# Kernel tuning notes

Measured on AMD Instinct MI355X. Metric: run time of the kernel, lower is better.

## Reference

```python
import jax, jax.numpy as jnp
import numpy as np

HID, NBINS = 256, 4
NMIR, NMRNA, B, NP, PD = 2000, 20000, 16, 2048, 1024
EREG, EPM, EPI = 300000, 320000, 32000


def _lin(x, w, b):
    return x @ w.T + b


def _gelu(x):
    # torch nn.GELU default = exact erf formulation
    return jax.nn.gelu(x, approximate=False)


def _ln(x, g, b):
    m = jnp.mean(x, axis=-1, keepdims=True)
    v = jnp.mean((x - m) ** 2, axis=-1, keepdims=True)
    return (x - m) * jax.lax.rsqrt(v + 1e-5) * g + b


def setup_inputs() -> dict:
    key = jax.random.key(0)
    ks = jax.random.split(key, 48)

    def lin_w(i, dout, din):
        s = 1.0 / np.sqrt(din)
        return jax.random.uniform(ks[i], (dout, din), minval=-s, maxval=s, dtype=jnp.float32)

    inp = {}
    inp['emb_mirna'] = jax.random.normal(ks[0], (NMIR, HID), jnp.float32) * 0.02
    inp['emb_mrna'] = jax.random.normal(ks[1], (NMRNA, HID), jnp.float32) * 0.02
    inp['w_mir2mrna'] = jax.random.uniform(ks[2], (EREG,), jnp.float32)
    inp['w_mrna2mir'] = jax.random.uniform(ks[3], (EREG,), jnp.float32)
    inp['w_mrna2pat'] = jax.random.uniform(ks[4], (EPM,), jnp.float32)
    inp['w_mir2pat'] = jax.random.uniform(ks[5], (EPI,), jnp.float32)
    inp['reg_w_mrna'] = lin_w(6, HID, HID)
    inp['reg_b_mrna'] = jnp.zeros((HID,), jnp.float32)
    inp['reg_w_mirna'] = lin_w(7, HID, HID)
    inp['reg_b_mirna'] = jnp.zeros((HID,), jnp.float32)
    inp['proj_w'] = lin_w(8, HID, HID)
    inp['proj_b'] = jnp.zeros((HID,), jnp.float32)
    inp['ln_g'] = jnp.ones((HID,), jnp.float32)
    inp['ln_b'] = jnp.zeros((HID,), jnp.float32)
    inp['omics_w'] = lin_w(9, NBINS, HID)
    inp['omics_b'] = jnp.zeros((NBINS,), jnp.float32)
    inp['wsi_w'] = lin_w(10, HID, PD)
    inp['wsi_b'] = jnp.zeros((HID,), jnp.float32)
    inp['mlp_w'] = lin_w(11, HID, HID)
    inp['mlp_b'] = jnp.zeros((HID,), jnp.float32)
    inp['wln_g'] = jnp.ones((HID,), jnp.float32)
    inp['wln_b'] = jnp.zeros((HID,), jnp.float32)
    inp['fuse_w1'] = lin_w(12, HID, 2 * HID)
    inp['fuse_b1'] = jnp.zeros((HID,), jnp.float32)
    inp['fuse_w2'] = lin_w(13, NBINS, HID)
    inp['fuse_b2'] = jnp.zeros((NBINS,), jnp.float32)
    inp['patches'] = jax.random.normal(ks[14], (B, NP, PD), jnp.float32)
    inp['mask'] = jnp.ones((B, NP), jnp.float32)
    inp['src_mir2mrna'] = jax.random.randint(ks[15], (EREG,), 0, NMIR, jnp.int32)
    inp['dst_mir2mrna'] = jax.random.randint(ks[16], (EREG,), 0, NMRNA, jnp.int32)
    inp['src_mrna2mir'] = jax.random.randint(ks[17], (EREG,), 0, NMRNA, jnp.int32)
    inp['dst_mrna2mir'] = jax.random.randint(ks[18], (EREG,), 0, NMIR, jnp.int32)
    inp['src_mrna2pat'] = jax.random.randint(ks[19], (EPM,), 0, NMRNA, jnp.int32)
    inp['dst_mrna2pat'] = jax.random.randint(ks[20], (EPM,), 0, B, jnp.int32)
    inp['src_mir2pat'] = jax.random.randint(ks[21], (EPI,), 0, NMIR, jnp.int32)
    inp['dst_mir2pat'] = jax.random.randint(ks[22], (EPI,), 0, B, jnp.int32)
    return inp


def reference(emb_mirna, emb_mrna, w_mir2mrna, w_mrna2mir, w_mrna2pat, w_mir2pat,
              reg_w_mrna, reg_b_mrna, reg_w_mirna, reg_b_mirna,
              proj_w, proj_b, ln_g, ln_b, omics_w, omics_b,
              wsi_w, wsi_b, mlp_w, mlp_b, wln_g, wln_b,
              fuse_w1, fuse_b1, fuse_w2, fuse_b2, patches, mask,
              src_mir2mrna, dst_mir2mrna, src_mrna2mir, dst_mrna2mir,
              src_mrna2pat, dst_mrna2pat, src_mir2pat, dst_mir2pat):
    # ---- omics: node embeddings (nid = arange -> full tables) ----
    h_mir, h_mrna = emb_mirna, emb_mrna
    # ---- SimpleRegEncoder: weighted gather-scatter-sum per etype (on ORIGINAL h) ----
    agg_mrna = jax.ops.segment_sum(h_mir[src_mir2mrna] * w_mir2mrna[:, None], dst_mir2mrna, num_segments=NMRNA)
    agg_mir = jax.ops.segment_sum(h_mrna[src_mrna2mir] * w_mrna2mir[:, None], dst_mrna2mir, num_segments=NMIR)
    h_mrna = h_mrna + _gelu(_lin(agg_mrna, reg_w_mrna, reg_b_mrna))  # dropout = identity (eval)
    h_mir = h_mir + _gelu(_lin(agg_mir, reg_w_mirna, reg_b_mirna))
    # ---- PatientReadout: cross_reducer='sum' over both gene->patient etypes ----
    acc = (jax.ops.segment_sum(h_mrna[src_mrna2pat] * w_mrna2pat[:, None], dst_mrna2pat, num_segments=B)
           + jax.ops.segment_sum(h_mir[src_mir2pat] * w_mir2pat[:, None], dst_mir2pat, num_segments=B))
    pat = _ln(_gelu(_lin(acc, proj_w, proj_b)), ln_g, ln_b)  # [B, HID]
    omics_logits = _lin(pat, omics_w, omics_b)  # [B, NBINS]
    # ---- SimpleWSIEncoder ----
    x = _lin(patches, wsi_w, wsi_b)  # [B, NP, HID]
    denom = jnp.clip(jnp.sum(mask, axis=1, keepdims=True), 1.0, None)
    pooled = jnp.sum(x * mask[:, :, None], axis=1) / denom
    pooled = _gelu(_lin(_gelu(pooled), mlp_w, mlp_b))
    wsi = _ln(pooled, wln_g, wln_b)  # [B, HID]
    # ---- fusion head ----
    cat = jnp.concatenate([pat, wsi], axis=-1)  # [B, 2*HID]
    fused = _lin(_gelu(_lin(cat, fuse_w1, fuse_b1)), fuse_w2, fuse_b2)  # [B, NBINS]
    return fused, omics_logits
```

## Files before the change

### kernel.cpp

```cpp
#include <hip/hip_runtime.h>
#include <math.h>

#define HID 256
#define NBINS 4
#define NMIR 2000
#define NMRNA 20000
#define NG (NMRNA + NMIR)
#define BB 16
#define NP 2048
#define PD 1024
#define EREG 300000
#define EPM 320000
#define EPI 32000

typedef __attribute__((ext_vector_type(8))) short bf16x8;
typedef __attribute__((ext_vector_type(4))) float f32x4;

__device__ __forceinline__ float gelu_exact(float x) {
    return 0.5f * x * (1.0f + erff(x * 0.7071067811865475f));
}

__device__ __forceinline__ unsigned short f2b(float f) {
    union { float f; unsigned int u; } v; v.f = f;
    unsigned int u = v.u + 0x7fffu + ((v.u >> 16) & 1u);
    return (unsigned short)(u >> 16);
}

__device__ __forceinline__ float b2f(unsigned short u) {
    union { unsigned int i; float f; } v; v.i = ((unsigned int)u) << 16;
    return v.f;
}

__device__ __forceinline__ float block_reduce_sum(float v, float* red) {
    int c = threadIdx.x;
    red[c] = v;
    __syncthreads();
    for (int st = 128; st > 0; st >>= 1) {
        if (c < st) red[c] += red[c + st];
        __syncthreads();
    }
    float r = red[0];
    __syncthreads();
    return r;
}

__device__ __forceinline__ float kred(float v, float* red, int b, int kk) {
    red[kk * 16 + b] = v;
    __syncthreads();
    for (int st = 8; st >= 1; st >>= 1) {
        if (kk < st) red[kk * 16 + b] += red[(kk + st) * 16 + b];
        __syncthreads();
    }
    float r = red[b];
    __syncthreads();
    return r;
}

#define CVT_EMB ((NG * HID) / 4096)
#define CVT_F2B ((2 * HID * HID) / 4096)
#define CVT_TOTAL (CVT_EMB + CVT_F2B)

__global__ __launch_bounds__(256) void k_cvt(
        const float* __restrict__ emb_mirna, const float* __restrict__ emb_mrna,
        unsigned short* __restrict__ embB_mir, unsigned short* __restrict__ embB_mrna,
        const float* __restrict__ regwA, const float* __restrict__ regwB,
        unsigned short* __restrict__ wb) {
    int bid = blockIdx.x;
    int t = threadIdx.x;
    if (bid < CVT_EMB) {
        const size_t NM = (size_t)NMIR * HID;
        float4 v[4];
#pragma unroll
        for (int k = 0; k < 4; k++) {
            size_t e = (size_t)bid * 4096 + k * 1024 + t * 4;
            v[k] = (e < NM) ? *(const float4*)(emb_mirna + e)
                            : *(const float4*)(emb_mrna + (e - NM));
        }
#pragma unroll
        for (int k = 0; k < 4; k++) {
            size_t e = (size_t)bid * 4096 + k * 1024 + t * 4;
            ushort4 u = { f2b(v[k].x), f2b(v[k].y), f2b(v[k].z), f2b(v[k].w) };
            if (e < NM) *(ushort4*)(embB_mir + e) = u;
            else        *(ushort4*)(embB_mrna + (e - NM)) = u;
        }
        return;
    }
    bid -= CVT_EMB;
    {
        const size_t NW = (size_t)HID * HID;
        float4 v[4];
#pragma unroll
        for (int k = 0; k < 4; k++) {
            size_t e = (size_t)bid * 4096 + k * 1024 + t * 4;
            v[k] = (e < NW) ? *(const float4*)(regwA + e)
                            : *(const float4*)(regwB + (e - NW));
        }
#pragma unroll
        for (int k = 0; k < 4; k++) {
            size_t e = (size_t)bid * 4096 + k * 1024 + t * 4;
            ushort4 u = { f2b(v[k].x), f2b(v[k].y), f2b(v[k].z), f2b(v[k].w) };
            *(ushort4*)(wb + e) = u;
        }
    }
}

#define NBR 128
#define NBP 32
#define PER_R ((2 * EREG + NBR - 1) / NBR)
#define PER_P ((EPM + EPI + NBP - 1) / NBP)

__global__ __launch_bounds__(1024) void k_hist(
        const int* __restrict__ dR1, const int* __restrict__ dR2,
        const int* __restrict__ sP1, const int* __restrict__ sP2,
        int* __restrict__ histR, int* __restrict__ histP) {
    __shared__ int lh[NG];
    int t = threadIdx.x, bid = blockIdx.x;
    for (int i = t; i < NG; i += 1024) lh[i] = 0;
    __syncthreads();
    if (bid < NBR) {
        int beg = bid * PER_R, end = min(beg + PER_R, 2 * EREG);
        for (int i = beg + t; i < end; i += 1024) {
            int d = (i < EREG) ? dR1[i] : NMRNA + dR2[i - EREG];
            atomicAdd(&lh[d], 1);
        }
        __syncthreads();
        int* out = histR + (size_t)bid * NG;
        for (int i = t; i < NG; i += 1024) out[i] = lh[i];
    } else {
        int pb = bid - NBR;
        int beg = pb * PER_P, end = min(beg + PER_P, EPM + EPI);
        for (int i = beg + t; i < end; i += 1024) {
            int g = (i < EPM) ? sP1[i] : NMRNA + sP2[i - EPM];
            atomicAdd(&lh[g], 1);
        }
        __syncthreads();
        int* out = histP + (size_t)pb * NG;
        for (int i = t; i < NG; i += 1024) out[i] = lh[i];
    }
}

#define CS_B ((NG + 255) / 256)
__global__ __launch_bounds__(256) void k_colsum(
        const int* __restrict__ histR, const int* __restrict__ histP,
        int* __restrict__ baseR, int* __restrict__ baseP,
        int* __restrict__ cntR, int* __restrict__ cntP) {
    int bid = blockIdx.x;
    if (bid < CS_B) {
        int i = bid * 256 + threadIdx.x;
        if (i >= NG) return;
        int run = 0;
        for (int b = 0; b < NBR; b++) {
            baseR[(size_t)b * NG + i] = run;
            run += histR[(size_t)b * NG + i];
        }
        cntR[i] = run;
    } else {
        int i = (bid - CS_B) * 256 + threadIdx.x;
        if (i >= NG) return;
        int run = 0;
        for (int b = 0; b < NBP; b++) {
            baseP[(size_t)b * NG + i] = run;
            run += histP[(size_t)b * NG + i];
        }
        cntP[i] = run;
    }
}

__global__ __launch_bounds__(1024) void k_scan_small(
        const int* __restrict__ cntR, const int* __restrict__ cntP,
        int* __restrict__ rowptrR, int* __restrict__ rowptrP) {
    __shared__ int part[1024];
    const int* cnt = blockIdx.x ? cntP : cntR;
    int* rowptr = blockIdx.x ? rowptrP : rowptrR;
    int t = threadIdx.x;
    const int chunk = (NG + 1023) >> 10;
    int beg = t * chunk, end = min(beg + chunk, NG);
    int s = 0;
    for (int i = beg; i < end; i++) s += cnt[i];
    part[t] = s;
    __syncthreads();
    for (int st = 1; st < 1024; st <<= 1) {
        int v = (t >= st) ? part[t - st] : 0;
        __syncthreads();
        part[t] += v;
        __syncthreads();
    }
    int off = part[t] - s;
    for (int i = beg; i < end; i++) {
        rowptr[i] = off;
        off += cnt[i];
    }
    if (end == NG) rowptr[NG] = off;
}

__global__ __launch_bounds__(1024) void k_place(
        const int* __restrict__ sR1, const int* __restrict__ dR1, const float* __restrict__ wR1,
        const int* __restrict__ sR2, const int* __restrict__ dR2, const float* __restrict__ wR2,
        const int* __restrict__ sP1, const int* __restrict__ dP1, const float* __restrict__ wP1,
        const int* __restrict__ sP2, const int* __restrict__ dP2, const float* __restrict__ wP2,
        const int* __restrict__ baseR, const int* __restrict__ baseP,
        const int* __restrict__ rowptrR, const int* __restrict__ rowptrP,
        int2* __restrict__ epR, int2* __restrict__ epP) {
    __shared__ int lcur[NG];
    int t = threadIdx.x, bid = blockIdx.x;
    if (bid < NBR) {
        const int* base = baseR + (size_t)bid * NG;
        for (int i = t; i < NG; i += 1024) lcur[i] = rowptrR[i] + base[i];
        __syncthreads();
        int beg = bid * PER_R, end = min(beg + PER_R, 2 * EREG);
        for (int i = beg + t; i < end; i += 1024) {
            int d, s; float w;
            if (i < EREG) { d = dR1[i]; s = sR1[i]; w = wR1[i]; }
            else { int k = i - EREG; d = NMRNA + dR2[k]; s = sR2[k]; w = wR2[k]; }
            int p = atomicAdd(&lcur[d], 1);
            int2 e; e.x = s; e.y = __float_as_int(w);
            epR[p] = e;
        }
    } else {
        int pb = bid - NBR;
        const int* base = baseP + (size_t)pb * NG;
        for (int i = t; i < NG; i += 1024) lcur[i] = rowptrP[i] + base[i];
        __syncthreads();
        int beg = pb * PER_P, end = min(beg + PER_P, EPM + EPI);
        for (int i = beg + t; i < end; i += 1024) {
            int g, b; float w;
            if (i < EPM) { g = sP1[i]; b = dP1[i]; w = wP1[i]; }
            else { int k = i - EPM; g = NMRNA + sP2[k]; b = dP2[k]; w = wP2[k]; }
            int p = atomicAdd(&lcur[g], 1);
            int2 e; e.x = (g << 4) | b; e.y = __float_as_int(w);
            epP[p] = e;
        }
    }
}

#define PSLICES 128
#define PCHUNK (NP / PSLICES)
__global__ __launch_bounds__(256) void k_pool(
        const float* __restrict__ patches, const float* __restrict__ mask,
        float* __restrict__ pooled, float* __restrict__ masksum) {
    int b = blockIdx.y;
    int p0 = blockIdx.x * PCHUNK;
    int t = threadIdx.x;
    float4 acc = {0.f, 0.f, 0.f, 0.f};
    float msum = 0.f;
#pragma unroll
    for (int pp = 0; pp < PCHUNK; pp++) {
        int p = p0 + pp;
        float m = mask[b * NP + p];
        float4 v = ((const float4*)(patches + ((size_t)b * NP + p) * PD))[t];
        msum += m;
        acc.x += m * v.x; acc.y += m * v.y; acc.z += m * v.z; acc.w += m * v.w;
    }
    float* op = pooled + (size_t)b * PD + t * 4;
    atomicAdd(op + 0, acc.x);
    atomicAdd(op + 1, acc.y);
    atomicAdd(op + 2, acc.z);
    atomicAdd(op + 3, acc.w);
    if (t == 0) atomicAdd(&masksum[b], msum);
}

__global__ __launch_bounds__(256) void k_gather2(
        const unsigned short* __restrict__ embB_mir, const unsigned short* __restrict__ embB_mrna,
        const int* __restrict__ rowptrR, const int2* __restrict__ epR,
        unsigned short* __restrict__ agg) {
    __shared__ float lacc[4][HID];
    int n = blockIdx.x;
    const unsigned short* emb = (n < NMRNA) ? embB_mir : embB_mrna;
    int wv = threadIdx.x >> 6, l = threadIdx.x & 63;
    int beg = rowptrR[n], end = rowptrR[n + 1];
    float a0 = 0.f, a1 = 0.f, a2 = 0.f, a3 = 0.f;
    float c0 = 0.f, c1 = 0.f, c2 = 0.f, c3 = 0.f;
    float d0 = 0.f, d1 = 0.f, d2 = 0.f, d3 = 0.f;
    float g0 = 0.f, g1 = 0.f, g2 = 0.f, g3 = 0.f;
    int j = beg + wv;
    for (; j + 12 < end; j += 16) {
        int2 e0 = epR[j];
        int2 e1 = epR[j + 4];
        int2 e2 = epR[j + 8];
        int2 e3 = epR[j + 12];
        float w0 = __int_as_float(e0.y), w1 = __int_as_float(e1.y);
        float w2 = __int_as_float(e2.y), w3 = __int_as_float(e3.y);
        ushort4 v0 = *(const ushort4*)(emb + (size_t)e0.x * HID + l * 4);
        ushort4 v1 = *(const ushort4*)(emb + (size_t)e1.x * HID + l * 4);
        ushort4 v2 = *(const ushort4*)(emb + (size_t)e2.x * HID + l * 4);
        ushort4 v3 = *(const ushort4*)(emb + (size_t)e3.x * HID + l * 4);
        a0 += w0 * b2f(v0.x); a1 += w0 * b2f(v0.y); a2 += w0 * b2f(v0.z); a3 += w0 * b2f(v0.w);
        c0 += w1 * b2f(v1.x); c1 += w1 * b2f(v1.y); c2 += w1 * b2f(v1.z); c3 += w1 * b2f(v1.w);
        d0 += w2 * b2f(v2.x); d1 += w2 * b2f(v2.y); d2 += w2 * b2f(v2.z); d3 += w2 * b2f(v2.w);
        g0 += w3 * b2f(v3.x); g1 += w3 * b2f(v3.y); g2 += w3 * b2f(v3.z); g3 += w3 * b2f(v3.w);
    }
    for (; j < end; j += 4) {
        int2 e0 = epR[j];
        float w0 = __int_as_float(e0.y);
        ushort4 v0 = *(const ushort4*)(emb + (size_t)e0.x * HID + l * 4);
        a0 += w0 * b2f(v0.x); a1 += w0 * b2f(v0.y); a2 += w0 * b2f(v0.z); a3 += w0 * b2f(v0.w);
    }
    float4 st = { a0 + c0 + d0 + g0, a1 + c1 + d1 + g1,
                  a2 + c2 + d2 + g2, a3 + c3 + d3 + g3 };
    ((float4*)lacc[wv])[l] = st;
    __syncthreads();
    int c = threadIdx.x;
    agg[(size_t)n * HID + c] = f2b(lacc[0][c] + lacc[1][c] + lacc[2][c] + lacc[3][c]);
}

__global__ __launch_bounds__(256) void k_update2(
        const unsigned short* __restrict__ A,
        const float* __restrict__ emb_mrna, const float* __restrict__ emb_mirna,
        const unsigned short* __restrict__ wb,
        const float* __restrict__ bias_mrna, const float* __restrict__ bias_mirna,
        const int* __restrict__ rowptrP, const int2* __restrict__ epP,
        float* __restrict__ acc_pat) {
    __shared__ float ht[16][HID + 1];
    __shared__ float wtile[16][BB];
    int row0 = blockIdx.x * 16;
    const float* emb; const unsigned short* Wb; const float* bias; int base;
    if (row0 < NMRNA) { emb = emb_mrna;  Wb = wb;             bias = bias_mrna;  base = 0; }
    else              { emb = emb_mirna; Wb = wb + HID * HID; bias = bias_mirna; base = NMRNA; }
    int tid = threadIdx.x;
    if (tid < 16 * BB) wtile[tid >> 4][tid & 15] = 0.f;
    __syncthreads();
    int pbeg = rowptrP[row0], pend = rowptrP[row0 + 16];
    for (int j = pbeg + tid; j < pend; j += 256) {
        int2 e = epP[j];
        atomicAdd(&wtile[(e.x >> 4) - row0][e.x & 15], __int_as_float(e.y));
    }
    int wv = tid >> 6;
    int lane = tid & 63;
    int m = lane & 15;
    int q = lane >> 4;
    bf16x8 afrag[8];
    const unsigned short* arow = A + (size_t)(row0 + m) * HID + q * 8;
#pragma unroll
    for (int kk = 0; kk < 8; kk++)
        afrag[kk] = *(const bf16x8*)(arow + kk * 32);
    f32x4 acc[4];
#pragma unroll
    for (int t = 0; t < 4; t++) acc[t] = (f32x4){0.f, 0.f, 0.f, 0.f};
    int col_base = wv * 64;
#pragma unroll
    for (int t = 0; t < 4; t++) {
        const unsigned short* brow = Wb + (size_t)(col_base + t * 16 + m) * HID + q * 8;
#pragma unroll
        for (int kk = 0; kk < 8; kk++) {
            bf16x8 bfrag = *(const bf16x8*)(brow + kk * 32);
            acc[t] = __builtin_amdgcn_mfma_f32_16x16x32_bf16(afrag[kk], bfrag, acc[t], 0, 0, 0);
        }
    }
#pragma unroll
    for (int t = 0; t < 4; t++) {
        int col = col_base + t * 16 + m;
        float bv = bias[col];
#pragma unroll
        for (int r = 0; r < 4; r++) {
            int lrow = q * 4 + r;
            size_t idxe = (size_t)(row0 - base + lrow) * HID + col;
            ht[lrow][col] = emb[idxe] + gelu_exact(acc[t][r] + bv);
        }
    }
    __syncthreads();
    int c = tid;
    float hv[16];
#pragma unroll
    for (int r = 0; r < 16; r++) hv[r] = ht[r][c];
#pragma unroll
    for (int b = 0; b < BB; b++) {
        float s = 0.f;
#pragma unroll
        for (int r = 0; r < 16; r++) s += wtile[r][b] * hv[r];
        atomicAdd(&acc_pat[b * HID + c], s);
    }
}

__global__ __launch_bounds__(256) void k_head_a(
        const float* __restrict__ acc_pat, const float* __restrict__ pooled,
        const float* __restrict__ masksum,
        const float* __restrict__ proj_w, const float* __restrict__ proj_b,
        const float* __restrict__ wsi_w, const float* __restrict__ wsi_b,
        float* __restrict__ pg, float* __restrict__ wt) {
    __shared__ float red[256];
    int c = blockIdx.x;
    int t = threadIdx.x;
    int b = t & 15, kk = t >> 4;

    const float* wr = proj_w + (size_t)c * HID + kk * 16;
    const float* xr = acc_pat + (size_t)b * HID + kk * 16;
    float s = 0.f;
#pragma unroll
    for (int i = 0; i < 16; i += 4) {
        float4 w4 = *(const float4*)(wr + i);
        float4 x4 = *(const float4*)(xr + i);
        s += x4.x * w4.x + x4.y * w4.y + x4.z * w4.z + x4.w * w4.w;
    }
    float tot = kred(s, red, b, kk);
    if (kk == 0) pg[(size_t)b * HID + c] = gelu_exact(tot + proj_b[c]);

    const float* wr2 = wsi_w + (size_t)c * PD + kk * 64;
    const float* xr2 = pooled + (size_t)b * PD + kk * 64;
    float s2 = 0.f;
#pragma unroll
    for (int i = 0; i < 64; i += 4) {
        float4 w4 = *(const float4*)(wr2 + i);
        float4 x4 = *(const float4*)(xr2 + i);
        s2 += x4.x * w4.x + x4.y * w4.y + x4.z * w4.z + x4.w * w4.w;
    }
    float tot2 = kred(s2, red, b, kk);
    if (kk == 0) {
        float sm = masksum[b];
        float denom = fmaxf(sm, 1.0f);
        wt[(size_t)b * HID + c] = gelu_exact(tot2 / denom + wsi_b[c] * (sm / denom));
    }
}

__global__ __launch_bounds__(256) void k_head_b(
        const float* __restrict__ wt,
        const float* __restrict__ mlp_w, const float* __restrict__ mlp_b,
        float* __restrict__ ml) {
    __shared__ float red[256];
    int c = blockIdx.x;
    int t = threadIdx.x;
    int b = t & 15, kk = t >> 4;
    const float* wr = mlp_w + (size_t)c * HID + kk * 16;
    const float* xr = wt + (size_t)b * HID + kk * 16;
    float s = 0.f;
#pragma unroll
    for (int i = 0; i < 16; i += 4) {
        float4 w4 = *(const float4*)(wr + i);
        float4 x4 = *(const float4*)(xr + i);
        s += x4.x * w4.x + x4.y * w4.y + x4.z * w4.z + x4.w * w4.w;
    }
    float tot = kred(s, red, b, kk);
    if (kk == 0) ml[(size_t)b * HID + c] = gelu_exact(tot + mlp_b[c]);
}

__global__ __launch_bounds__(256) void k_head_c(
        const float* __restrict__ pg, const float* __restrict__ ml,
        const float* __restrict__ ln_g, const float* __restrict__ ln_b,
        const float* __restrict__ wln_g, const float* __restrict__ wln_b,
        const float* __restrict__ omics_w, const float* __restrict__ omics_b,
        const float* __restrict__ fuse_b2,
        float* __restrict__ vecbuf, float* __restrict__ out_omics,
        float* __restrict__ out_fused) {
    __shared__ float red[256];
    int b = blockIdx.x, c = threadIdx.x;
    if (c < NBINS) out_fused[b * NBINS + c] = fuse_b2[c];
    float g = pg[(size_t)b * HID + c];
    float mean = block_reduce_sum(g, red) * (1.0f / HID);
    float d = g - mean;
    float var = block_reduce_sum(d * d, red) * (1.0f / HID);
    float patv = d * rsqrtf(var + 1e-5f) * ln_g[c] + ln_b[c];
    vecbuf[(size_t)b * (2 * HID) + c] = patv;
    for (int o = 0; o < NBINS; o++) {
        float r = block_reduce_sum(patv * omics_w[o * HID + c], red);
        if (c == 0) out_omics[b * NBINS + o] = r + omics_b[o];
    }
    float m = ml[(size_t)b * HID + c];
    mean = block_reduce_sum(m, red) * (1.0f / HID);
    d = m - mean;
    var = block_reduce_sum(d * d, red) * (1.0f / HID);
    vecbuf[(size_t)b * (2 * HID) + HID + c] = d * rsqrtf(var + 1e-5f) * wln_g[c] + wln_b[c];
}

__global__ __launch_bounds__(256) void k_head_d(
        const float* __restrict__ vecbuf,
        const float* __restrict__ fuse_w1, const float* __restrict__ fuse_b1,
        const float* __restrict__ fuse_w2,
        float* __restrict__ out_fused) {
    __shared__ float red[256];
    int c = blockIdx.x;
    int t = threadIdx.x;
    int b = t & 15, kk = t >> 4;
    const float* wr = fuse_w1 + (size_t)c * (2 * HID) + kk * 32;
    const float* xr = vecbuf + (size_t)b * (2 * HID) + kk * 32;
    float s = 0.f;
#pragma unroll
    for (int i = 0; i < 32; i += 4) {
        float4 w4 = *(const float4*)(wr + i);
        float4 x4 = *(const float4*)(xr + i);
        s += x4.x * w4.x + x4.y * w4.y + x4.z * w4.z + x4.w * w4.w;
    }
    float tot = kred(s, red, b, kk);
    if (kk == 0) {
        float h1 = gelu_exact(tot + fuse_b1[c]);
#pragma unroll
        for (int o = 0; o < NBINS; o++)
            atomicAdd(&out_fused[b * NBINS + o], h1 * fuse_w2[o * HID + c]);
    }
}

extern "C" void kernel_launch(void* const* d_in, const int* in_sizes, int n_in,
                              void* d_out, int out_size, void* d_ws, size_t ws_size,
                              hipStream_t stream) {
    const float* emb_mirna  = (const float*)d_in[0];
    const float* emb_mrna   = (const float*)d_in[1];
    const float* w_mir2mrna = (const float*)d_in[2];
    const float* w_mrna2mir = (const float*)d_in[3];
    const float* w_mrna2pat = (const float*)d_in[4];
    const float* w_mir2pat  = (const float*)d_in[5];
    const float* reg_w_mrna = (const float*)d_in[6];
    const float* reg_b_mrna = (const float*)d_in[7];
    const float* reg_w_mirna= (const float*)d_in[8];
    const float* reg_b_mirna= (const float*)d_in[9];
    const float* proj_w     = (const float*)d_in[10];
    const float* proj_b     = (const float*)d_in[11];
    const float* ln_g       = (const float*)d_in[12];
    const float* ln_b       = (const float*)d_in[13];
    const float* omics_w    = (const float*)d_in[14];
    const float* omics_b    = (const float*)d_in[15];
    const float* wsi_w      = (const float*)d_in[16];
    const float* wsi_b      = (const float*)d_in[17];
    const float* mlp_w      = (const float*)d_in[18];
    const float* mlp_b      = (const float*)d_in[19];
    const float* wln_g      = (const float*)d_in[20];
    const float* wln_b      = (const float*)d_in[21];
    const float* fuse_w1    = (const float*)d_in[22];
    const float* fuse_b1    = (const float*)d_in[23];
    const float* fuse_w2    = (const float*)d_in[24];
    const float* fuse_b2    = (const float*)d_in[25];
    const float* patches    = (const float*)d_in[26];
    const float* mask       = (const float*)d_in[27];
    const int* src_m2M = (const int*)d_in[28];
    const int* dst_m2M = (const int*)d_in[29];
    const int* src_M2m = (const int*)d_in[30];
    const int* dst_M2m = (const int*)d_in[31];
    const int* src_M2p = (const int*)d_in[32];
    const int* dst_M2p = (const int*)d_in[33];
    const int* src_m2p = (const int*)d_in[34];
    const int* dst_m2p = (const int*)d_in[35];

    float* ws = (float*)d_ws;
    size_t off = 0;
    float* acc_pat  = ws + off; off += (size_t)BB * HID;
    float* pooled   = ws + off; off += (size_t)BB * PD;
    float* masksum  = ws + off; off += BB;
    size_t zero_floats = off;
    unsigned short* agg_bf = (unsigned short*)(ws + off); off += (size_t)NG * HID / 2;
    unsigned short* wb     = (unsigned short*)(ws + off); off += (size_t)2 * HID * HID / 2;
    unsigned short* embB_mir  = (unsigned short*)(ws + off); off += (size_t)NMIR * HID / 2;
    unsigned short* embB_mrna = (unsigned short*)(ws + off); off += (size_t)NMRNA * HID / 2;
    float* pg       = ws + off; off += (size_t)BB * HID;
    float* wt       = ws + off; off += (size_t)BB * HID;
    float* ml       = ws + off; off += (size_t)BB * HID;
    float* vecbuf   = ws + off; off += (size_t)BB * 2 * HID;
    int* histR      = (int*)(ws + off); off += (size_t)NBR * NG;
    int* histP      = (int*)(ws + off); off += (size_t)NBP * NG;
    int* baseR      = (int*)(ws + off); off += (size_t)NBR * NG;
    int* baseP      = (int*)(ws + off); off += (size_t)NBP * NG;
    int* cntR       = (int*)(ws + off); off += NG;
    int* cntP       = (int*)(ws + off); off += NG;
    int* rowptrR    = (int*)(ws + off); off += NG + 2;
    int* rowptrP    = (int*)(ws + off); off += NG + 2;
    int2* epR       = (int2*)(ws + off); off += (size_t)2 * (2 * EREG);
    int2* epP       = (int2*)(ws + off); off += (size_t)2 * (EPM + EPI);

    float* out_fused = (float*)d_out;
    float* out_omics = (float*)d_out + BB * NBINS;

    hipMemsetAsync(d_ws, 0, zero_floats * sizeof(float), stream);

    k_cvt<<<CVT_TOTAL, 256, 0, stream>>>(
        emb_mirna, emb_mrna, embB_mir, embB_mrna,
        reg_w_mrna, reg_w_mirna, wb);

    k_hist<<<NBR + NBP, 1024, 0, stream>>>(
        dst_m2M, dst_M2m, src_M2p, src_m2p, histR, histP);
    k_colsum<<<2 * CS_B, 256, 0, stream>>>(histR, histP, baseR, baseP, cntR, cntP);
    k_scan_small<<<2, 1024, 0, stream>>>(cntR, cntP, rowptrR, rowptrP);
    k_place<<<NBR + NBP, 1024, 0, stream>>>(
        src_m2M, dst_m2M, w_mir2mrna, src_M2m, dst_M2m, w_mrna2mir,
        src_M2p, dst_M2p, w_mrna2pat, src_m2p, dst_m2p, w_mir2pat,
        baseR, baseP, rowptrR, rowptrP, epR, epP);

    k_pool<<<dim3(PSLICES, BB), 256, 0, stream>>>(patches, mask, pooled, masksum);

    k_gather2<<<NG, 256, 0, stream>>>(embB_mir, embB_mrna, rowptrR, epR, agg_bf);

    k_update2<<<NG / 16, 256, 0, stream>>>(agg_bf, emb_mrna, emb_mirna, wb,
                                           reg_b_mrna, reg_b_mirna,
                                           rowptrP, epP, acc_pat);

    k_head_a<<<HID, 256, 0, stream>>>(acc_pat, pooled, masksum,
                                      proj_w, proj_b, wsi_w, wsi_b, pg, wt);
    k_head_b<<<HID, 256, 0, stream>>>(wt, mlp_w, mlp_b, ml);
    k_head_c<<<BB, 256, 0, stream>>>(pg, ml, ln_g, ln_b, wln_g, wln_b,
                                     omics_w, omics_b, fuse_b2,
                                     vecbuf, out_omics, out_fused);
    k_head_d<<<HID, 256, 0, stream>>>(vecbuf, fuse_w1, fuse_b1, fuse_w2, out_fused);
}
```

Before: 533.3 us.

## Merge pooling, bf16 conversion and histogram into one front kernel

Folds the patch mask-pooling, the embedding/weight bf16 conversion and the edge-degree histogram into a single launch with block-range dispatch, so the large bandwidth-bound pooling read runs alongside the histogram and conversion work. The histogram now packs two 16-bit counters per shared int, halving the shared footprint so more 1024-thread blocks fit per CU. Packed counters overflow if any node receives more than 65535 edges in one block's range, and the conversion blocks now use 1024 threads with one float4 each.

```diff
diff --git a/kernel.cpp b/kernel.cpp
--- a/kernel.cpp
+++ b/kernel.cpp
@@ -56,86 +56,98 @@
     return r;
 }
 
-#define CVT_EMB ((NG * HID) / 4096)
-#define CVT_F2B ((2 * HID * HID) / 4096)
-#define CVT_TOTAL (CVT_EMB + CVT_F2B)
-
-__global__ __launch_bounds__(256) void k_cvt(
-        const float* __restrict__ emb_mirna, const float* __restrict__ emb_mrna,
-        unsigned short* __restrict__ embB_mir, unsigned short* __restrict__ embB_mrna,
-        const float* __restrict__ regwA, const float* __restrict__ regwB,
-        unsigned short* __restrict__ wb) {
-    int bid = blockIdx.x;
-    int t = threadIdx.x;
-    if (bid < CVT_EMB) {
-        const size_t NM = (size_t)NMIR * HID;
-        float4 v[4];
-#pragma unroll
-        for (int k = 0; k < 4; k++) {
-            size_t e = (size_t)bid * 4096 + k * 1024 + t * 4;
-            v[k] = (e < NM) ? *(const float4*)(emb_mirna + e)
-                            : *(const float4*)(emb_mrna + (e - NM));
-        }
-#pragma unroll
-        for (int k = 0; k < 4; k++) {
-            size_t e = (size_t)bid * 4096 + k * 1024 + t * 4;
-            ushort4 u = { f2b(v[k].x), f2b(v[k].y), f2b(v[k].z), f2b(v[k].w) };
-            if (e < NM) *(ushort4*)(embB_mir + e) = u;
-            else        *(ushort4*)(embB_mrna + (e - NM)) = u;
-        }
-        return;
-    }
-    bid -= CVT_EMB;
-    {
-        const size_t NW = (size_t)HID * HID;
-        float4 v[4];
-#pragma unroll
-        for (int k = 0; k < 4; k++) {
-            size_t e = (size_t)bid * 4096 + k * 1024 + t * 4;
-            v[k] = (e < NW) ? *(const float4*)(regwA + e)
-                            : *(const float4*)(regwB + (e - NW));
-        }
-#pragma unroll
-        for (int k = 0; k < 4; k++) {
-            size_t e = (size_t)bid * 4096 + k * 1024 + t * 4;
-            ushort4 u = { f2b(v[k].x), f2b(v[k].y), f2b(v[k].z), f2b(v[k].w) };
-            *(ushort4*)(wb + e) = u;
-        }
-    }
-}
-
 #define NBR 128
 #define NBP 32
 #define PER_R ((2 * EREG + NBR - 1) / NBR)
 #define PER_P ((EPM + EPI + NBP - 1) / NBP)
 
-__global__ __launch_bounds__(1024) void k_hist(
+#define FR_POOL 512
+#define FR_EMB ((NG * HID) / 4096)
+#define FR_F2B ((2 * HID * HID) / 4096)
+#define FR_TOTAL (FR_POOL + FR_EMB + FR_F2B + NBR + NBP)
+
+__global__ __launch_bounds__(1024) void k_front(
+        const float* __restrict__ patches, const float* __restrict__ mask,
+        float* __restrict__ pooled, float* __restrict__ masksum,
+        const float* __restrict__ emb_mirna, const float* __restrict__ emb_mrna,
+        unsigned short* __restrict__ embB_mir, unsigned short* __restrict__ embB_mrna,
+        const float* __restrict__ regwA, const float* __restrict__ regwB,
+        unsigned short* __restrict__ wb,
         const int* __restrict__ dR1, const int* __restrict__ dR2,
         const int* __restrict__ sP1, const int* __restrict__ sP2,
         int* __restrict__ histR, int* __restrict__ histP) {
-    __shared__ int lh[NG];
-    int t = threadIdx.x, bid = blockIdx.x;
-    for (int i = t; i < NG; i += 1024) lh[i] = 0;
+    __shared__ int lh[NG / 2];
+    int bid = blockIdx.x;
+    int t = threadIdx.x;
+    if (bid < FR_POOL) {
+        int slice = bid & 31, b = bid >> 5;
+        int sub = t >> 8, col = t & 255;
+        int p0 = slice * 64 + sub * 16;
+        float4 acc = {0.f, 0.f, 0.f, 0.f};
+        float msum = 0.f;
+#pragma unroll
+        for (int pp = 0; pp < 16; pp++) {
+            int p = p0 + pp;
+            float m = mask[b * NP + p];
+            float4 v = ((const float4*)(patches + ((size_t)b * NP + p) * PD))[col];
+            msum += m;
+            acc.x += m * v.x; acc.y += m * v.y; acc.z += m * v.z; acc.w += m * v.w;
+        }
+        float* op = pooled + (size_t)b * PD + col * 4;
+        atomicAdd(op + 0, acc.x);
+        atomicAdd(op + 1, acc.y);
+        atomicAdd(op + 2, acc.z);
+        atomicAdd(op + 3, acc.w);
+        if (col == 0) atomicAdd(&masksum[b], msum);
+        return;
+    }
+    bid -= FR_POOL;
+    if (bid < FR_EMB) {
+        const size_t NM = (size_t)NMIR * HID;
+        size_t e = (size_t)bid * 4096 + t * 4;
+        float4 v;
+        unsigned short* o;
+        if (e < NM) { v = *(const float4*)(emb_mirna + e); o = embB_mir + e; }
+        else        { v = *(const float4*)(emb_mrna + (e - NM)); o = embB_mrna + (e - NM); }
+        ushort4 u = { f2b(v.x), f2b(v.y), f2b(v.z), f2b(v.w) };
+        *(ushort4*)o = u;
+        return;
+    }
+    bid -= FR_EMB;
+    if (bid < FR_F2B) {
+        const size_t NW = (size_t)HID * HID;
+        size_t e = (size_t)bid * 4096 + t * 4;
+        float4 v;
+        if (e < NW) v = *(const float4*)(regwA + e);
+        else v = *(const float4*)(regwB + (e - NW));
+        ushort4 u = { f2b(v.x), f2b(v.y), f2b(v.z), f2b(v.w) };
+        *(ushort4*)(wb + e) = u;
+        return;
+    }
+    bid -= FR_F2B;
+    for (int i = t; i < NG / 2; i += 1024) lh[i] = 0;
     __syncthreads();
     if (bid < NBR) {
         int beg = bid * PER_R, end = min(beg + PER_R, 2 * EREG);
         for (int i = beg + t; i < end; i += 1024) {
             int d = (i < EREG) ? dR1[i] : NMRNA + dR2[i - EREG];
-            atomicAdd(&lh[d], 1);
+            atomicAdd(&lh[d >> 1], 1u << ((d & 1) << 4));
         }
         __syncthreads();
         int* out = histR + (size_t)bid * NG;
-        for (int i = t; i < NG; i += 1024) out[i] = lh[i];
+        for (int i = t; i < NG; i += 1024)
+            out[i] = (lh[i >> 1] >> ((i & 1) << 4)) & 0xFFFF;
     } else {
         int pb = bid - NBR;
         int beg = pb * PER_P, end = min(beg + PER_P, EPM + EPI);
         for (int i = beg + t; i < end; i += 1024) {
             int g = (i < EPM) ? sP1[i] : NMRNA + sP2[i - EPM];
-            atomicAdd(&lh[g], 1);
+            atomicAdd(&lh[g >> 1], 1u << ((g & 1) << 4));
         }
         __syncthreads();
         int* out = histP + (size_t)pb * NG;
-        for (int i = t; i < NG; i += 1024) out[i] = lh[i];
+        for (int i = t; i < NG; i += 1024)
+            out[i] = (lh[i >> 1] >> ((i & 1) << 4)) & 0xFFFF;
     }
 }
 
@@ -231,32 +243,6 @@
             epP[p] = e;
         }
     }
-}
-
-#define PSLICES 128
-#define PCHUNK (NP / PSLICES)
-__global__ __launch_bounds__(256) void k_pool(
-        const float* __restrict__ patches, const float* __restrict__ mask,
-        float* __restrict__ pooled, float* __restrict__ masksum) {
-    int b = blockIdx.y;
-    int p0 = blockIdx.x * PCHUNK;
-    int t = threadIdx.x;
-    float4 acc = {0.f, 0.f, 0.f, 0.f};
-    float msum = 0.f;
-#pragma unroll
-    for (int pp = 0; pp < PCHUNK; pp++) {
-        int p = p0 + pp;
-        float m = mask[b * NP + p];
-        float4 v = ((const float4*)(patches + ((size_t)b * NP + p) * PD))[t];
-        msum += m;
-        acc.x += m * v.x; acc.y += m * v.y; acc.z += m * v.z; acc.w += m * v.w;
-    }
-    float* op = pooled + (size_t)b * PD + t * 4;
-    atomicAdd(op + 0, acc.x);
-    atomicAdd(op + 1, acc.y);
-    atomicAdd(op + 2, acc.z);
-    atomicAdd(op + 3, acc.w);
-    if (t == 0) atomicAdd(&masksum[b], msum);
 }
 
 __global__ __launch_bounds__(256) void k_gather2(
@@ -557,20 +543,18 @@
 
     hipMemsetAsync(d_ws, 0, zero_floats * sizeof(float), stream);
 
-    k_cvt<<<CVT_TOTAL, 256, 0, stream>>>(
+    k_front<<<FR_TOTAL, 1024, 0, stream>>>(
+        patches, mask, pooled, masksum,
         emb_mirna, emb_mrna, embB_mir, embB_mrna,
-        reg_w_mrna, reg_w_mirna, wb);
-
-    k_hist<<<NBR + NBP, 1024, 0, stream>>>(
+        reg_w_mrna, reg_w_mirna, wb,
         dst_m2M, dst_M2m, src_M2p, src_m2p, histR, histP);
+
     k_colsum<<<2 * CS_B, 256, 0, stream>>>(histR, histP, baseR, baseP, cntR, cntP);
     k_scan_small<<<2, 1024, 0, stream>>>(cntR, cntP, rowptrR, rowptrP);
     k_place<<<NBR + NBP, 1024, 0, stream>>>(
         src_m2M, dst_m2M, w_mir2mrna, src_M2m, dst_M2m, w_mrna2mir,
         src_M2p, dst_M2p, w_mrna2pat, src_m2p, dst_m2p, w_mir2pat,
         baseR, baseP, rowptrR, rowptrP, epR, epP);
-
-    k_pool<<<dim3(PSLICES, BB), 256, 0, stream>>>(patches, mask, pooled, masksum);
 
     k_gather2<<<NG, 256, 0, stream>>>(embB_mir, embB_mrna, rowptrR, epR, agg_bf);
 
```

Measured after the change: 519.0 us. 1.03x faster.
